# Optimization experiments

Measured on AMD Instinct MI355X. Metric: run time of the kernel, lower is better.

## Reference

```python
import jax, jax.numpy as jnp
import numpy as np

B, T, C, H = 2, 2048, 1024, 16
HD = C // H  # head dim = 64


def setup_inputs() -> dict:
    key = jax.random.key(0)
    ks = jax.random.split(key, 5)
    s = 1.0 / np.sqrt(C)
    return {
        "x": jax.random.normal(ks[0], (B, T, C), dtype=jnp.float32),
        "Wq": jax.random.normal(ks[1], (C, C), dtype=jnp.float32) * s,
        "bq": jnp.zeros((C,), dtype=jnp.float32),
        "Wk": jax.random.normal(ks[2], (C, C), dtype=jnp.float32) * s,
        "bk": jnp.zeros((C,), dtype=jnp.float32),
        "Wv": jax.random.normal(ks[3], (C, C), dtype=jnp.float32) * s,
        "bv": jnp.zeros((C,), dtype=jnp.float32),
        "Wp": jax.random.normal(ks[4], (C, C), dtype=jnp.float32) * s,
        "bp": jnp.zeros((C,), dtype=jnp.float32),
    }


def reference(x, Wq, bq, Wk, bk, Wv, bv, Wp, bp):
    # QKV projections -> [B, H, T, HD]
    def proj(W, b):
        return (x @ W.T + b).reshape(B, T, H, HD).transpose(0, 2, 1, 3)

    q = proj(Wq, bq)
    k = proj(Wk, bk)
    v = proj(Wv, bv)

    scale = 1.0 / np.sqrt(HD)
    att = jnp.einsum("bhtd,bhsd->bhts", q, k) * scale  # [B,H,T,T]
    causal = jnp.tril(jnp.ones((T, T), dtype=bool))
    att = jnp.where(causal, att, -jnp.inf)
    att = jax.nn.softmax(att, axis=-1)
    y = jnp.einsum("bhts,bhsd->bhtd", att, v)          # [B,H,T,HD]
    y = y.transpose(0, 2, 1, 3).reshape(B, T, C)
    return y @ Wp.T + bp
```

## Files before the change

### kernel.cpp

```cpp
#include <hip/hip_runtime.h>
#include <hip/hip_bf16.h>

#define BB 2
#define TT 2048
#define CC 1024
#define HH 16
#define HDD 64

typedef __attribute__((ext_vector_type(8))) short bf16x8;
typedef __attribute__((ext_vector_type(4))) float f32x4;

static __device__ __forceinline__ unsigned short f2bf(float f) {
  union { float f; unsigned u; } v; v.f = f;
  unsigned r = v.u + 0x7fffu + ((v.u >> 16) & 1u);
  return (unsigned short)(r >> 16);
}

static __device__ __forceinline__ unsigned fbits(float f) {
  union { float f; unsigned u; } v; v.f = f; return v.u;
}

static __device__ __forceinline__ unsigned pk_trunc(float lo, float hi) {
  return __builtin_amdgcn_perm(fbits(hi), fbits(lo), 0x07060302u);
}

static __device__ __forceinline__ float fexp2(float x) {
#if __has_builtin(__builtin_amdgcn_exp2f)
  return __builtin_amdgcn_exp2f(x);
#else
  return exp2f(x);
#endif
}

static __device__ __forceinline__ void gload_lds16(const unsigned short* g, unsigned short* l) {
  __builtin_amdgcn_global_load_lds((const __attribute__((address_space(1))) void*)g,
                                   (__attribute__((address_space(3))) void*)l, 16, 0, 0);
}

__global__ __launch_bounds__(256) void convert_all(
    const float* __restrict__ x, const float* __restrict__ Wq,
    const float* __restrict__ Wk, const float* __restrict__ Wv,
    const float* __restrict__ Wp, unsigned short* __restrict__ dst)
{
  const size_t M4 = 4194304, M1 = 1048576;
  const size_t e = ((size_t)blockIdx.x * 256 + threadIdx.x) * 8;
  const float* src; size_t off;
  if (e < M4)            { src = x;  off = e; }
  else if (e < M4 + M1)  { src = Wq; off = e - M4; }
  else if (e < M4 + 2*M1){ src = Wk; off = e - M4 - M1; }
  else if (e < M4 + 3*M1){ src = Wv; off = e - M4 - 2*M1; }
  else                   { src = Wp; off = e - M4 - 3*M1; }
  float4 a = *(const float4*)(src + off);
  float4 c = *(const float4*)(src + off + 4);
  unsigned short buf[8] = {f2bf(a.x), f2bf(a.y), f2bf(a.z), f2bf(a.w),
                           f2bf(c.x), f2bf(c.y), f2bf(c.z), f2bf(c.w)};
  *(uint4*)(dst + e) = *(const uint4*)buf;
}

__global__ __launch_bounds__(256) void gemm_mfma(
    const unsigned short* __restrict__ A, const unsigned short* __restrict__ W,
    const float* __restrict__ b0, const float* __restrict__ b1, const float* __restrict__ b2,
    unsigned short* __restrict__ oQ, unsigned short* __restrict__ oK,
    unsigned short* __restrict__ oVt)
{
  __shared__ unsigned short As[128][32];
  __shared__ unsigned short Bs[128][32];
  const int t = threadIdx.x;
  const int wv = __builtin_amdgcn_readfirstlane(t >> 6);
  const int ln = t & 63;
  const int l16 = ln & 15;
  const int quad = ln >> 4;
  const int mBase = blockIdx.x * 128;
  const int nBase = blockIdx.y * 128;
  const int wm = (wv >> 1) * 64, wn = (wv & 1) * 64;

  f32x4 acc[4][4];
#pragma unroll
  for (int i = 0; i < 4; i++)
#pragma unroll
    for (int j = 0; j < 4; j++) acc[i][j] = (f32x4){0.f, 0.f, 0.f, 0.f};

  const int ca = wv * 64 + ln;
  const int cb = ca + 256;
  const int ra = ca >> 2, colA = (ca & 3) * 8;
  const int rb = cb >> 2, colB = (cb & 3) * 8;
  unsigned short* ldsA0 = &As[0][0] + (size_t)(wv * 64) * 8;
  unsigned short* ldsA1 = &As[0][0] + (size_t)(256 + wv * 64) * 8;
  unsigned short* ldsB0 = &Bs[0][0] + (size_t)(wv * 64) * 8;
  unsigned short* ldsB1 = &Bs[0][0] + (size_t)(256 + wv * 64) * 8;
  const unsigned short* apA0 = A + (size_t)(mBase + ra) * CC + colA;
  const unsigned short* apA1 = A + (size_t)(mBase + rb) * CC + colB;
  const unsigned short* apB0 = W + (size_t)(nBase + ra) * CC + colA;
  const unsigned short* apB1 = W + (size_t)(nBase + rb) * CC + colB;

  for (int kb = 0; kb < CC; kb += 32) {
    __syncthreads();
    gload_lds16(apA0 + kb, ldsA0);
    gload_lds16(apA1 + kb, ldsA1);
    gload_lds16(apB0 + kb, ldsB0);
    gload_lds16(apB1 + kb, ldsB1);
    __syncthreads();
    bf16x8 af[4], bfr[4];
#pragma unroll
    for (int i = 0; i < 4; i++) af[i] = *(const bf16x8*)&As[wm + i * 16 + l16][quad * 8];
#pragma unroll
    for (int j = 0; j < 4; j++) bfr[j] = *(const bf16x8*)&Bs[wn + j * 16 + l16][quad * 8];
#pragma unroll
    for (int i = 0; i < 4; i++)
#pragma unroll
      for (int j = 0; j < 4; j++)
        acc[i][j] = __builtin_amdgcn_mfma_f32_16x16x32_bf16(af[i], bfr[j], acc[i][j], 0, 0, 0);
  }

  const int which = nBase >> 10;
  const float* bias = which == 0 ? b0 : (which == 1 ? b1 : b2);
  unsigned short* dst = which == 0 ? oQ : (which == 1 ? oK : oVt);
  const float scl = which == 0 ? 0.1803368801f : 1.0f;
#pragma unroll
  for (int i = 0; i < 4; i++)
#pragma unroll
    for (int r = 0; r < 4; r++) {
      const int m = mBase + wm + i * 16 + quad * 4 + r;
      const int b = m >> 11, tp = m & 2047;
#pragma unroll
      for (int j = 0; j < 4; j++) {
        const int n = nBase + wn + j * 16 + l16;
        const int nl = n & 1023, h = nl >> 6, d = nl & 63;
        const unsigned short v = f2bf((acc[i][j][r] + bias[nl]) * scl);
        if (which < 2) dst[((size_t)(b * HH + h) * TT + tp) * HDD + d] = v;
        else           dst[((size_t)(b * HH + h) * HDD + d) * TT + tp] = v;
      }
    }
}

__global__ __launch_bounds__(512) void gemm_proj(
    const unsigned short* __restrict__ A, const unsigned short* __restrict__ W,
    const float* __restrict__ bias, float* __restrict__ out)
{
  __shared__ unsigned short As[128][32];
  __shared__ unsigned short Bs[128][32];
  const int t = threadIdx.x;
  const int wv = __builtin_amdgcn_readfirstlane(t >> 6);
  const int ln = t & 63;
  const int l16 = ln & 15;
  const int quad = ln >> 4;
  const int mBase = blockIdx.x * 128;
  const int nBase = blockIdx.y * 128;
  const int wm = (wv >> 2) * 64;
  const int wn = (wv & 3) * 32;

  f32x4 acc[4][2];
#pragma unroll
  for (int i = 0; i < 4; i++)
#pragma unroll
    for (int j = 0; j < 2; j++) acc[i][j] = (f32x4){0.f, 0.f, 0.f, 0.f};

  const int rs = t >> 2, cs = (t & 3) * 8;
  unsigned short* ldsA = &As[0][0] + (size_t)t * 8;
  unsigned short* ldsB = &Bs[0][0] + (size_t)t * 8;
  const unsigned short* apA = A + (size_t)(mBase + rs) * CC + cs;
  const unsigned short* apB = W + (size_t)(nBase + rs) * CC + cs;

  for (int kb = 0; kb < CC; kb += 32) {
    __syncthreads();
    gload_lds16(apA + kb, ldsA);
    gload_lds16(apB + kb, ldsB);
    __syncthreads();
    bf16x8 af[4], bfr[2];
#pragma unroll
    for (int i = 0; i < 4; i++) af[i] = *(const bf16x8*)&As[wm + i * 16 + l16][quad * 8];
#pragma unroll
    for (int j = 0; j < 2; j++) bfr[j] = *(const bf16x8*)&Bs[wn + j * 16 + l16][quad * 8];
#pragma unroll
    for (int i = 0; i < 4; i++)
#pragma unroll
      for (int j = 0; j < 2; j++)
        acc[i][j] = __builtin_amdgcn_mfma_f32_16x16x32_bf16(af[i], bfr[j], acc[i][j], 0, 0, 0);
  }

#pragma unroll
  for (int i = 0; i < 4; i++)
#pragma unroll
    for (int r = 0; r < 4; r++) {
      const int m = mBase + wm + i * 16 + quad * 4 + r;
#pragma unroll
      for (int j = 0; j < 2; j++) {
        const int n = nBase + wn + j * 16 + l16;
        out[(size_t)m * CC + n] = acc[i][j][r] + bias[n];
      }
    }
}

__global__ __launch_bounds__(256, 2) void attn_mfma(
    const unsigned short* __restrict__ Q, const unsigned short* __restrict__ K,
    const unsigned short* __restrict__ Vt, unsigned short* __restrict__ y)
{
  __shared__ unsigned short QP[128][72];
  __shared__ unsigned short Ks[2][64][72];
  __shared__ unsigned short Vts[2][64][72];

  const int t = threadIdx.x;
  const int a = blockIdx.x;
  const int bh = blockIdx.y;
  const int wave = t >> 6;
  const int lane = t & 63;
  const int l16 = lane & 15;
  const int quad = lane >> 4;

  const size_t base = (size_t)bh * TT * HDD;
  const int qtL = a, qtH = 31 - a;
  const int qBaseL = qtL * 64, qBaseH = qtH * 64;

#pragma unroll
  for (int p = 0; p < 4; p++) {
    const int c = p * 256 + t;
    const int r = c >> 3, off = (c & 7) * 8;
    const int srcRow = (r < 64) ? (qBaseL + r) : (qBaseH + r - 64);
    *(uint4*)&QP[r][off] = *(const uint4*)(Q + base + (size_t)srcRow * HDD + off);
  }

  const int sr = t >> 2, sc = (t & 3) * 8;
  const unsigned short* kbase = K + base + (size_t)sr * HDD + sc;
  const unsigned short* vbase = Vt + base + (size_t)sr * TT + sc;
  uint4 kr0 = *(const uint4*)(kbase);
  uint4 kr1 = *(const uint4*)(kbase + 32);
  uint4 vr0 = *(const uint4*)(vbase);
  uint4 vr1 = *(const uint4*)(vbase + 32);
  __syncthreads();

  bf16x8 qfL0 = *(const bf16x8*)&QP[wave * 16 + l16][quad * 8];
  bf16x8 qfL1 = *(const bf16x8*)&QP[wave * 16 + l16][32 + quad * 8];
  bf16x8 qfH0 = *(const bf16x8*)&QP[64 + wave * 16 + l16][quad * 8];
  bf16x8 qfH1 = *(const bf16x8*)&QP[64 + wave * 16 + l16][32 + quad * 8];
  unsigned short (*PtH)[72] = (unsigned short (*)[72])&QP[wave * 16];
  unsigned short (*PtL)[72] = (unsigned short (*)[72])&QP[64 + wave * 16];

  float lL = 0.f, lH = 0.f;
  f32x4 OfrL[4], OfrH[4];
#pragma unroll
  for (int dt = 0; dt < 4; dt++) {
    OfrL[dt] = (f32x4){0.f, 0.f, 0.f, 0.f};
    OfrH[dt] = (f32x4){0.f, 0.f, 0.f, 0.f};
  }

  for (int kt = 0; kt <= qtH; kt++) {
    const int buf = kt & 1;
    *(uint4*)&Ks[buf][sr][sc]       = kr0;
    *(uint4*)&Ks[buf][sr][sc + 32]  = kr1;
    *(uint4*)&Vts[buf][sr][sc]      = vr0;
    *(uint4*)&Vts[buf][sr][sc + 32] = vr1;
    __syncthreads();
    if (kt < qtH) {
      kr0 = *(const uint4*)(kbase + (size_t)(kt + 1) * 64 * HDD);
      kr1 = *(const uint4*)(kbase + (size_t)(kt + 1) * 64 * HDD + 32);
      vr0 = *(const uint4*)(vbase + (kt + 1) * 64);
      vr1 = *(const uint4*)(vbase + (kt + 1) * 64 + 32);
    }
    const bool doLo = (kt <= qtL);

    f32x4 StH[4], StL[4];
#pragma unroll
    for (int ct = 0; ct < 4; ct++) {
      bf16x8 a0 = *(const bf16x8*)&Ks[buf][ct * 16 + l16][quad * 8];
      bf16x8 a1 = *(const bf16x8*)&Ks[buf][ct * 16 + l16][32 + quad * 8];
      f32x4 s = (f32x4){0.f, 0.f, 0.f, 0.f};
      s = __builtin_amdgcn_mfma_f32_16x16x32_bf16(a0, qfH0, s, 0, 0, 0);
      s = __builtin_amdgcn_mfma_f32_16x16x32_bf16(a1, qfH1, s, 0, 0, 0);
      StH[ct] = s;
      if (doLo) {
        f32x4 s2 = (f32x4){0.f, 0.f, 0.f, 0.f};
        s2 = __builtin_amdgcn_mfma_f32_16x16x32_bf16(a0, qfL0, s2, 0, 0, 0);
        s2 = __builtin_amdgcn_mfma_f32_16x16x32_bf16(a1, qfL1, s2, 0, 0, 0);
        StL[ct] = s2;
      }
    }

    if (kt == qtH) {
#pragma unroll
      for (int ct = 0; ct < 4; ct++) {
        float p[4];
#pragma unroll
        for (int r = 0; r < 4; r++) {
          float pv = fexp2(StH[ct][r]);
          if (ct * 16 + quad * 4 + r > wave * 16 + l16) pv = 0.f;
          p[r] = pv;
        }
        lH += (p[0] + p[1]) + (p[2] + p[3]);
        uint2 pk = {pk_trunc(p[0], p[1]), pk_trunc(p[2], p[3])};
        *(uint2*)&PtH[l16][ct * 16 + quad * 4] = pk;
      }
    } else {
#pragma unroll
      for (int ct = 0; ct < 4; ct++) {
        float p[4];
#pragma unroll
        for (int r = 0; r < 4; r++) p[r] = fexp2(StH[ct][r]);
        lH += (p[0] + p[1]) + (p[2] + p[3]);
        uint2 pk = {pk_trunc(p[0], p[1]), pk_trunc(p[2], p[3])};
        *(uint2*)&PtH[l16][ct * 16 + quad * 4] = pk;
      }
    }
    if (doLo) {
      if (kt == qtL) {
#pragma unroll
        for (int ct = 0; ct < 4; ct++) {
          float p[4];
#pragma unroll
          for (int r = 0; r < 4; r++) {
            float pv = fexp2(StL[ct][r]);
            if (ct * 16 + quad * 4 + r > wave * 16 + l16) pv = 0.f;
            p[r] = pv;
          }
          lL += (p[0] + p[1]) + (p[2] + p[3]);
          uint2 pk = {pk_trunc(p[0], p[1]), pk_trunc(p[2], p[3])};
          *(uint2*)&PtL[l16][ct * 16 + quad * 4] = pk;
        }
      } else {
#pragma unroll
        for (int ct = 0; ct < 4; ct++) {
          float p[4];
#pragma unroll
          for (int r = 0; r < 4; r++) p[r] = fexp2(StL[ct][r]);
          lL += (p[0] + p[1]) + (p[2] + p[3]);
          uint2 pk = {pk_trunc(p[0], p[1]), pk_trunc(p[2], p[3])};
          *(uint2*)&PtL[l16][ct * 16 + quad * 4] = pk;
        }
      }
    }

    bf16x8 paH0 = *(const bf16x8*)&PtH[l16][quad * 8];
    bf16x8 paH1 = *(const bf16x8*)&PtH[l16][32 + quad * 8];
    bf16x8 paL0, paL1;
    if (doLo) {
      paL0 = *(const bf16x8*)&PtL[l16][quad * 8];
      paL1 = *(const bf16x8*)&PtL[l16][32 + quad * 8];
    }
#pragma unroll
    for (int dt = 0; dt < 4; dt++) {
      bf16x8 vb0 = *(const bf16x8*)&Vts[buf][dt * 16 + l16][quad * 8];
      bf16x8 vb1 = *(const bf16x8*)&Vts[buf][dt * 16 + l16][32 + quad * 8];
      OfrH[dt] = __builtin_amdgcn_mfma_f32_16x16x32_bf16(paH0, vb0, OfrH[dt], 0, 0, 0);
      OfrH[dt] = __builtin_amdgcn_mfma_f32_16x16x32_bf16(paH1, vb1, OfrH[dt], 0, 0, 0);
      if (doLo) {
        OfrL[dt] = __builtin_amdgcn_mfma_f32_16x16x32_bf16(paL0, vb0, OfrL[dt], 0, 0, 0);
        OfrL[dt] = __builtin_amdgcn_mfma_f32_16x16x32_bf16(paL1, vb1, OfrL[dt], 0, 0, 0);
      }
    }
  }

  lL += __shfl_xor(lL, 16, 64); lL += __shfl_xor(lL, 32, 64);
  lH += __shfl_xor(lH, 16, 64); lH += __shfl_xor(lH, 32, 64);

  const int b = bh >> 4, h = bh & 15;
  float lRowL[4], lRowH[4];
#pragma unroll
  for (int r = 0; r < 4; r++) {
    lRowL[r] = __shfl(lL, quad * 4 + r, 16);
    lRowH[r] = __shfl(lH, quad * 4 + r, 16);
  }
#pragma unroll
  for (int r = 0; r < 4; r++) {
    const int qL = qBaseL + wave * 16 + quad * 4 + r;
    const int qH = qBaseH + wave * 16 + quad * 4 + r;
    const float invL = 1.0f / lRowL[r];
    const float invH = 1.0f / lRowH[r];
    unsigned short* ypL = y + ((size_t)(b * TT + qL)) * CC + h * 64 + l16;
    unsigned short* ypH = y + ((size_t)(b * TT + qH)) * CC + h * 64 + l16;
#pragma unroll
    for (int dt = 0; dt < 4; dt++) {
      ypL[dt * 16] = f2bf(OfrL[dt][r] * invL);
      ypH[dt * 16] = f2bf(OfrH[dt][r] * invH);
    }
  }
}

extern "C" void kernel_launch(void* const* d_in, const int* in_sizes, int n_in,
                              void* d_out, int out_size, void* d_ws, size_t ws_size,
                              hipStream_t stream) {
  const float* x  = (const float*)d_in[0];
  const float* Wq = (const float*)d_in[1];
  const float* bq = (const float*)d_in[2];
  const float* Wk = (const float*)d_in[3];
  const float* bk = (const float*)d_in[4];
  const float* Wv = (const float*)d_in[5];
  const float* bv = (const float*)d_in[6];
  const float* Wp = (const float*)d_in[7];
  const float* bp = (const float*)d_in[8];

  const size_t M4 = 4194304, M1 = 1048576;
  unsigned short* xb   = (unsigned short*)d_ws;
  unsigned short* wqb  = xb + M4;
  unsigned short* wpb  = wqb + 3 * M1;
  unsigned short* wsQ  = wpb + M1;
  unsigned short* wsK  = wsQ + M4;
  unsigned short* wsVt = wsK + M4;
  unsigned short* yb   = wsVt + M4;

  convert_all<<<4096, 256, 0, stream>>>(x, Wq, Wk, Wv, Wp, xb);
  gemm_mfma<<<dim3(32, 24), 256, 0, stream>>>(xb, wqb, bq, bk, bv,
                                              wsQ, wsK, wsVt);
  attn_mfma<<<dim3(16, BB * HH), 256, 0, stream>>>(wsQ, wsK, wsVt, yb);
  gemm_proj<<<dim3(32, 8), 512, 0, stream>>>(yb, wpb, bp, (float*)d_out);
}
```

Before: 189.3 us.

## Double-buffer GEMM LDS tiles with BK=64, XOR swizzle, and shared core macro

```diff
diff --git a/kernel.cpp b/kernel.cpp
--- a/kernel.cpp
+++ b/kernel.cpp
@@ -57,60 +57,79 @@
   *(uint4*)(dst + e) = *(const uint4*)buf;
 }
 
+
+#define GEMM128_CORE(As, Bs, Aptr, Wptr)                                        \
+  const int t = threadIdx.x;                                                    \
+  const int wv = __builtin_amdgcn_readfirstlane(t >> 6);                        \
+  const int ln = t & 63;                                                        \
+  const int l16 = ln & 15;                                                      \
+  const int quad = ln >> 4;                                                     \
+  const int mBase = blockIdx.x * 128;                                           \
+  const int nBase = blockIdx.y * 128;                                           \
+  const int wm = (wv >> 1) * 64, wn = (wv & 1) * 64;                            \
+  f32x4 acc[4][4];                                                              \
+  _Pragma("unroll")                                                             \
+  for (int i = 0; i < 4; i++)                                                   \
+    _Pragma("unroll")                                                           \
+    for (int j = 0; j < 4; j++) acc[i][j] = (f32x4){0.f, 0.f, 0.f, 0.f};        \
+        \
+  const int rowLoc = wv * 8 + (ln >> 3);                                        \
+  const int csrc = ((ln & 7) ^ (ln >> 3)) * 8;                                  \
+  const unsigned short* gA = Aptr + (size_t)(mBase + rowLoc) * CC + csrc;       \
+  const unsigned short* gB = Wptr + (size_t)(nBase + rowLoc) * CC + csrc;       \
+  const int xq = l16 & 7;                                                       \
+  const int sw0 = (quad ^ xq) * 8;                                              \
+  const int sw1 = ((4 + quad) ^ xq) * 8;                                        \
+  STAGE(0, 0);                                                                  \
+  asm volatile("s_waitcnt vmcnt(0)" ::: "memory");                              \
+  __builtin_amdgcn_s_barrier();                                                 \
+  asm volatile("" ::: "memory");                                                \
+  for (int kt = 0; kt < CC / 64; ++kt) {                                        \
+    const int cur = kt & 1;                                                     \
+    if (kt < CC / 64 - 1) STAGE(cur ^ 1, kt + 1);                               \
+    bf16x8 af[2][4], bfr[2][4];                                                 \
+    _Pragma("unroll")                                                           \
+    for (int i = 0; i < 4; ++i) {                                               \
+      af[0][i]  = *(const bf16x8*)&As[cur][wm + i * 16 + l16][sw0];             \
+      af[1][i]  = *(const bf16x8*)&As[cur][wm + i * 16 + l16][sw1];             \
+      bfr[0][i] = *(const bf16x8*)&Bs[cur][wn + i * 16 + l16][sw0];             \
+      bfr[1][i] = *(const bf16x8*)&Bs[cur][wn + i * 16 + l16][sw1];             \
+    }                                                                           \
+    __builtin_amdgcn_s_setprio(1);                                              \
+    _Pragma("unroll")                                                           \
+    for (int kh = 0; kh < 2; ++kh)                                              \
+      _Pragma("unroll")                                                         \
+      for (int i = 0; i < 4; ++i)                                               \
+        _Pragma("unroll")                                                       \
+        for (int j = 0; j < 4; ++j)                                             \
+          acc[i][j] = __builtin_amdgcn_mfma_f32_16x16x32_bf16(                  \
+              af[kh][i], bfr[kh][j], acc[i][j], 0, 0, 0);                       \
+    __builtin_amdgcn_s_setprio(0);                                              \
+    asm volatile("s_waitcnt vmcnt(0)" ::: "memory");                            \
+    __builtin_amdgcn_s_barrier();                                               \
+    asm volatile("" ::: "memory");                                              \
+  }
+
 __global__ __launch_bounds__(256) void gemm_mfma(
     const unsigned short* __restrict__ A, const unsigned short* __restrict__ W,
     const float* __restrict__ b0, const float* __restrict__ b1, const float* __restrict__ b2,
     unsigned short* __restrict__ oQ, unsigned short* __restrict__ oK,
     unsigned short* __restrict__ oVt)
 {
-  __shared__ unsigned short As[128][32];
-  __shared__ unsigned short Bs[128][32];
-  const int t = threadIdx.x;
-  const int wv = __builtin_amdgcn_readfirstlane(t >> 6);
-  const int ln = t & 63;
-  const int l16 = ln & 15;
-  const int quad = ln >> 4;
-  const int mBase = blockIdx.x * 128;
-  const int nBase = blockIdx.y * 128;
-  const int wm = (wv >> 1) * 64, wn = (wv & 1) * 64;
-
-  f32x4 acc[4][4];
-#pragma unroll
-  for (int i = 0; i < 4; i++)
-#pragma unroll
-    for (int j = 0; j < 4; j++) acc[i][j] = (f32x4){0.f, 0.f, 0.f, 0.f};
-
-  const int ca = wv * 64 + ln;
-  const int cb = ca + 256;
-  const int ra = ca >> 2, colA = (ca & 3) * 8;
-  const int rb = cb >> 2, colB = (cb & 3) * 8;
-  unsigned short* ldsA0 = &As[0][0] + (size_t)(wv * 64) * 8;
-  unsigned short* ldsA1 = &As[0][0] + (size_t)(256 + wv * 64) * 8;
-  unsigned short* ldsB0 = &Bs[0][0] + (size_t)(wv * 64) * 8;
-  unsigned short* ldsB1 = &Bs[0][0] + (size_t)(256 + wv * 64) * 8;
-  const unsigned short* apA0 = A + (size_t)(mBase + ra) * CC + colA;
-  const unsigned short* apA1 = A + (size_t)(mBase + rb) * CC + colB;
-  const unsigned short* apB0 = W + (size_t)(nBase + ra) * CC + colA;
-  const unsigned short* apB1 = W + (size_t)(nBase + rb) * CC + colB;
-
-  for (int kb = 0; kb < CC; kb += 32) {
-    __syncthreads();
-    gload_lds16(apA0 + kb, ldsA0);
-    gload_lds16(apA1 + kb, ldsA1);
-    gload_lds16(apB0 + kb, ldsB0);
-    gload_lds16(apB1 + kb, ldsB1);
-    __syncthreads();
-    bf16x8 af[4], bfr[4];
-#pragma unroll
-    for (int i = 0; i < 4; i++) af[i] = *(const bf16x8*)&As[wm + i * 16 + l16][quad * 8];
-#pragma unroll
-    for (int j = 0; j < 4; j++) bfr[j] = *(const bf16x8*)&Bs[wn + j * 16 + l16][quad * 8];
-#pragma unroll
-    for (int i = 0; i < 4; i++)
-#pragma unroll
-      for (int j = 0; j < 4; j++)
-        acc[i][j] = __builtin_amdgcn_mfma_f32_16x16x32_bf16(af[i], bfr[j], acc[i][j], 0, 0, 0);
-  }
+  __shared__ unsigned short As[2][128][64];
+  __shared__ unsigned short Bs[2][128][64];
+#define STAGE(b, kt)                                                            \
+  do {                                                                          \
+    const size_t ko = (size_t)(kt) * 64;                                        \
+    _Pragma("unroll")                                                           \
+    for (int ii = 0; ii < 4; ++ii) {                                            \
+      gload_lds16(gA + ko + (size_t)ii * 32 * CC, &As[b][ii * 32 + wv * 8][0]); \
+      gload_lds16(gB + ko + (size_t)ii * 32 * CC, &Bs[b][ii * 32 + wv * 8][0]); \
+    }                                                                           \
+  } while (0)
+
+  GEMM128_CORE(As, Bs, A, W)
+#undef STAGE
 
   const int which = nBase >> 10;
   const float* bias = which == 0 ? b0 : (which == 1 ? b1 : b2);
@@ -133,50 +152,24 @@
     }
 }
 
-__global__ __launch_bounds__(512) void gemm_proj(
+__global__ __launch_bounds__(256) void gemm_proj(
     const unsigned short* __restrict__ A, const unsigned short* __restrict__ W,
     const float* __restrict__ bias, float* __restrict__ out)
 {
-  __shared__ unsigned short As[128][32];
-  __shared__ unsigned short Bs[128][32];
-  const int t = threadIdx.x;
-  const int wv = __builtin_amdgcn_readfirstlane(t >> 6);
-  const int ln = t & 63;
-  const int l16 = ln & 15;
-  const int quad = ln >> 4;
-  const int mBase = blockIdx.x * 128;
-  const int nBase = blockIdx.y * 128;
-  const int wm = (wv >> 2) * 64;
-  const int wn = (wv & 3) * 32;
-
-  f32x4 acc[4][2];
-#pragma unroll
-  for (int i = 0; i < 4; i++)
-#pragma unroll
-    for (int j = 0; j < 2; j++) acc[i][j] = (f32x4){0.f, 0.f, 0.f, 0.f};
-
-  const int rs = t >> 2, cs = (t & 3) * 8;
-  unsigned short* ldsA = &As[0][0] + (size_t)t * 8;
-  unsigned short* ldsB = &Bs[0][0] + (size_t)t * 8;
-  const unsigned short* apA = A + (size_t)(mBase + rs) * CC + cs;
-  const unsigned short* apB = W + (size_t)(nBase + rs) * CC + cs;
-
-  for (int kb = 0; kb < CC; kb += 32) {
-    __syncthreads();
-    gload_lds16(apA + kb, ldsA);
-    gload_lds16(apB + kb, ldsB);
-    __syncthreads();
-    bf16x8 af[4], bfr[2];
-#pragma unroll
-    for (int i = 0; i < 4; i++) af[i] = *(const bf16x8*)&As[wm + i * 16 + l16][quad * 8];
-#pragma unroll
-    for (int j = 0; j < 2; j++) bfr[j] = *(const bf16x8*)&Bs[wn + j * 16 + l16][quad * 8];
-#pragma unroll
-    for (int i = 0; i < 4; i++)
-#pragma unroll
-      for (int j = 0; j < 2; j++)
-        acc[i][j] = __builtin_amdgcn_mfma_f32_16x16x32_bf16(af[i], bfr[j], acc[i][j], 0, 0, 0);
-  }
+  __shared__ unsigned short As[2][128][64];
+  __shared__ unsigned short Bs[2][128][64];
+#define STAGE(b, kt)                                                            \
+  do {                                                                          \
+    const size_t ko = (size_t)(kt) * 64;                                        \
+    _Pragma("unroll")                                                           \
+    for (int ii = 0; ii < 4; ++ii) {                                            \
+      gload_lds16(gA + ko + (size_t)ii * 32 * CC, &As[b][ii * 32 + wv * 8][0]); \
+      gload_lds16(gB + ko + (size_t)ii * 32 * CC, &Bs[b][ii * 32 + wv * 8][0]); \
+    }                                                                           \
+  } while (0)
+
+  GEMM128_CORE(As, Bs, A, W)
+#undef STAGE
 
 #pragma unroll
   for (int i = 0; i < 4; i++)
@@ -184,7 +177,7 @@
     for (int r = 0; r < 4; r++) {
       const int m = mBase + wm + i * 16 + quad * 4 + r;
 #pragma unroll
-      for (int j = 0; j < 2; j++) {
+      for (int j = 0; j < 4; j++) {
         const int n = nBase + wn + j * 16 + l16;
         out[(size_t)m * CC + n] = acc[i][j][r] + bias[n];
       }
@@ -400,5 +393,5 @@
   gemm_mfma<<<dim3(32, 24), 256, 0, stream>>>(xb, wqb, bq, bk, bv,
                                               wsQ, wsK, wsVt);
   attn_mfma<<<dim3(16, BB * HH), 256, 0, stream>>>(wsQ, wsK, wsVt, yb);
-  gemm_proj<<<dim3(32, 8), 512, 0, stream>>>(yb, wpb, bp, (float*)d_out);
-}
+  gemm_proj<<<dim3(32, 8), 256, 0, stream>>>(yb, wpb, bp, (float*)d_out);
+}
```

After: 201.4 us. 1.06x slower.

## Double-buffer LDS tiles and swizzle layout in QKV and projection GEMMs

Applied to the files above, without the earlier changes.

```diff
diff --git a/kernel.cpp b/kernel.cpp
--- a/kernel.cpp
+++ b/kernel.cpp
@@ -57,14 +57,15 @@
   *(uint4*)(dst + e) = *(const uint4*)buf;
 }
 
+
 __global__ __launch_bounds__(256) void gemm_mfma(
     const unsigned short* __restrict__ A, const unsigned short* __restrict__ W,
     const float* __restrict__ b0, const float* __restrict__ b1, const float* __restrict__ b2,
     unsigned short* __restrict__ oQ, unsigned short* __restrict__ oK,
     unsigned short* __restrict__ oVt)
 {
-  __shared__ unsigned short As[128][32];
-  __shared__ unsigned short Bs[128][32];
+  __shared__ unsigned short As[2][128][32];
+  __shared__ unsigned short Bs[2][128][32];
   const int t = threadIdx.x;
   const int wv = __builtin_amdgcn_readfirstlane(t >> 6);
   const int ln = t & 63;
@@ -80,37 +81,49 @@
 #pragma unroll
     for (int j = 0; j < 4; j++) acc[i][j] = (f32x4){0.f, 0.f, 0.f, 0.f};
 
-  const int ca = wv * 64 + ln;
-  const int cb = ca + 256;
-  const int ra = ca >> 2, colA = (ca & 3) * 8;
-  const int rb = cb >> 2, colB = (cb & 3) * 8;
-  unsigned short* ldsA0 = &As[0][0] + (size_t)(wv * 64) * 8;
-  unsigned short* ldsA1 = &As[0][0] + (size_t)(256 + wv * 64) * 8;
-  unsigned short* ldsB0 = &Bs[0][0] + (size_t)(wv * 64) * 8;
-  unsigned short* ldsB1 = &Bs[0][0] + (size_t)(256 + wv * 64) * 8;
-  const unsigned short* apA0 = A + (size_t)(mBase + ra) * CC + colA;
-  const unsigned short* apA1 = A + (size_t)(mBase + rb) * CC + colB;
-  const unsigned short* apB0 = W + (size_t)(nBase + ra) * CC + colA;
-  const unsigned short* apB1 = W + (size_t)(nBase + rb) * CC + colB;
-
-  for (int kb = 0; kb < CC; kb += 32) {
-    __syncthreads();
-    gload_lds16(apA0 + kb, ldsA0);
-    gload_lds16(apA1 + kb, ldsA1);
-    gload_lds16(apB0 + kb, ldsB0);
-    gload_lds16(apB1 + kb, ldsB1);
-    __syncthreads();
+  const int rloc = t >> 2;
+  const int csrc = ((t & 3) ^ ((t >> 3) & 3)) * 8;
+  const unsigned short* gA = A + (size_t)(mBase + rloc) * CC + csrc;
+  const unsigned short* gB = W + (size_t)(nBase + rloc) * CC + csrc;
+  const int sw = (quad ^ ((l16 >> 1) & 3)) * 8;
+
+#define STAGE(b, kt)                                                       \
+  do {                                                                     \
+    const size_t ko = (size_t)(kt) * 32;                                   \
+    gload_lds16(gA + ko,               &As[b][0][0] + t * 8);              \
+    gload_lds16(gA + ko + 64 * CC,     &As[b][64][0] + t * 8);             \
+    gload_lds16(gB + ko,               &Bs[b][0][0] + t * 8);              \
+    gload_lds16(gB + ko + 64 * CC,     &Bs[b][64][0] + t * 8);             \
+  } while (0)
+
+  STAGE(0, 0);
+  for (int kt = 0; kt < 32; ++kt) {
+    const int cur = kt & 1;
+    if (kt < 31) {
+      STAGE(cur ^ 1, kt + 1);
+      asm volatile("s_waitcnt vmcnt(4)" ::: "memory");
+    } else {
+      asm volatile("s_waitcnt vmcnt(0)" ::: "memory");
+    }
+    __builtin_amdgcn_s_barrier();
+    asm volatile("" ::: "memory");
     bf16x8 af[4], bfr[4];
 #pragma unroll
-    for (int i = 0; i < 4; i++) af[i] = *(const bf16x8*)&As[wm + i * 16 + l16][quad * 8];
-#pragma unroll
-    for (int j = 0; j < 4; j++) bfr[j] = *(const bf16x8*)&Bs[wn + j * 16 + l16][quad * 8];
-#pragma unroll
-    for (int i = 0; i < 4; i++)
-#pragma unroll
-      for (int j = 0; j < 4; j++)
+    for (int i = 0; i < 4; ++i) af[i] = *(const bf16x8*)&As[cur][wm + i * 16 + l16][sw];
+#pragma unroll
+    for (int j = 0; j < 4; ++j) bfr[j] = *(const bf16x8*)&Bs[cur][wn + j * 16 + l16][sw];
+    __builtin_amdgcn_s_setprio(1);
+#pragma unroll
+    for (int i = 0; i < 4; ++i)
+#pragma unroll
+      for (int j = 0; j < 4; ++j)
         acc[i][j] = __builtin_amdgcn_mfma_f32_16x16x32_bf16(af[i], bfr[j], acc[i][j], 0, 0, 0);
-  }
+    __builtin_amdgcn_s_setprio(0);
+    asm volatile("" ::: "memory");
+    __builtin_amdgcn_s_barrier();
+    asm volatile("" ::: "memory");
+  }
+#undef STAGE
 
   const int which = nBase >> 10;
   const float* bias = which == 0 ? b0 : (which == 1 ? b1 : b2);
@@ -137,8 +150,8 @@
     const unsigned short* __restrict__ A, const unsigned short* __restrict__ W,
     const float* __restrict__ bias, float* __restrict__ out)
 {
-  __shared__ unsigned short As[128][32];
-  __shared__ unsigned short Bs[128][32];
+  __shared__ unsigned short As[2][128][32];
+  __shared__ unsigned short Bs[2][128][32];
   const int t = threadIdx.x;
   const int wv = __builtin_amdgcn_readfirstlane(t >> 6);
   const int ln = t & 63;
@@ -155,28 +168,47 @@
 #pragma unroll
     for (int j = 0; j < 2; j++) acc[i][j] = (f32x4){0.f, 0.f, 0.f, 0.f};
 
-  const int rs = t >> 2, cs = (t & 3) * 8;
-  unsigned short* ldsA = &As[0][0] + (size_t)t * 8;
-  unsigned short* ldsB = &Bs[0][0] + (size_t)t * 8;
-  const unsigned short* apA = A + (size_t)(mBase + rs) * CC + cs;
-  const unsigned short* apB = W + (size_t)(nBase + rs) * CC + cs;
-
-  for (int kb = 0; kb < CC; kb += 32) {
-    __syncthreads();
-    gload_lds16(apA + kb, ldsA);
-    gload_lds16(apB + kb, ldsB);
-    __syncthreads();
+  const int rloc = t >> 2;
+  const int csrc = ((t & 3) ^ ((t >> 3) & 3)) * 8;
+  const unsigned short* gA = A + (size_t)(mBase + rloc) * CC + csrc;
+  const unsigned short* gB = W + (size_t)(nBase + rloc) * CC + csrc;
+  const int sw = (quad ^ ((l16 >> 1) & 3)) * 8;
+
+#define STAGE(b, kt)                                                       \
+  do {                                                                     \
+    const size_t ko = (size_t)(kt) * 32;                                   \
+    gload_lds16(gA + ko, &As[b][0][0] + t * 8);                            \
+    gload_lds16(gB + ko, &Bs[b][0][0] + t * 8);                            \
+  } while (0)
+
+  STAGE(0, 0);
+  for (int kt = 0; kt < 32; ++kt) {
+    const int cur = kt & 1;
+    if (kt < 31) {
+      STAGE(cur ^ 1, kt + 1);
+      asm volatile("s_waitcnt vmcnt(2)" ::: "memory");
+    } else {
+      asm volatile("s_waitcnt vmcnt(0)" ::: "memory");
+    }
+    __builtin_amdgcn_s_barrier();
+    asm volatile("" ::: "memory");
     bf16x8 af[4], bfr[2];
 #pragma unroll
-    for (int i = 0; i < 4; i++) af[i] = *(const bf16x8*)&As[wm + i * 16 + l16][quad * 8];
-#pragma unroll
-    for (int j = 0; j < 2; j++) bfr[j] = *(const bf16x8*)&Bs[wn + j * 16 + l16][quad * 8];
-#pragma unroll
-    for (int i = 0; i < 4; i++)
-#pragma unroll
-      for (int j = 0; j < 2; j++)
+    for (int i = 0; i < 4; ++i) af[i] = *(const bf16x8*)&As[cur][wm + i * 16 + l16][sw];
+#pragma unroll
+    for (int j = 0; j < 2; ++j) bfr[j] = *(const bf16x8*)&Bs[cur][wn + j * 16 + l16][sw];
+    __builtin_amdgcn_s_setprio(1);
+#pragma unroll
+    for (int i = 0; i < 4; ++i)
+#pragma unroll
+      for (int j = 0; j < 2; ++j)
         acc[i][j] = __builtin_amdgcn_mfma_f32_16x16x32_bf16(af[i], bfr[j], acc[i][j], 0, 0, 0);
-  }
+    __builtin_amdgcn_s_setprio(0);
+    asm volatile("" ::: "memory");
+    __builtin_amdgcn_s_barrier();
+    asm volatile("" ::: "memory");
+  }
+#undef STAGE
 
 #pragma unroll
   for (int i = 0; i < 4; i++)
```

Result: no change. 187.1 us (-1.1%).
